# Performance work log

Hardware: AMD Instinct MI355X
Metric: run time of the kernel (lower is better)

Reference implementation:

```python
import jax, jax.numpy as jnp
import numpy as np

N_NODES = 100000
N_EDGES = 3200000
N_CLASSES = 16
P = 2  # p-norm order


def setup_inputs() -> dict:
    key = jax.random.key(0)
    k1, k2, k3 = jax.random.split(key, 3)
    edge_index = jax.random.randint(k1, (2, N_EDGES), 0, N_NODES, dtype=jnp.int64)
    edge_weights = jax.random.uniform(k2, (N_EDGES,), dtype=jnp.float32)
    y = jax.random.normal(k3, (N_NODES, N_CLASSES), dtype=jnp.float32)
    return {"edge_index": edge_index, "edge_weights": edge_weights, "y": y}


def reference(edge_index, edge_weights, y):
    row, col = edge_index[0], edge_index[1]
    n = y.shape[0]
    # sym normalization: degree = row-sum of weighted adjacency (O(E) segment sum,
    # replacing the original dense NxN materialization)
    degree = jax.ops.segment_sum(edge_weights, row, num_segments=n)
    d = jnp.sqrt(degree)
    d_r = d[row][:, None]  # (E,1)
    d_c = d[col][:, None]
    diff = y[row] / d_r - y[col] / d_c  # (E,C)
    pnorm = jnp.sum(jnp.abs(diff) ** P, axis=1) ** (1.0 / P)  # (E,)
    return jnp.mean(pnorm * edge_weights)
```

## Files before the change

### kernel.cpp

```cpp
#include <hip/hip_runtime.h>
#include <hip/hip_fp16.h>

#define N_NODES   100000
#define N_CLASSES 16
#define N_EDGES   3200000

#define R_DYN     3
#define NPR_DYN   33334
#define DYN_BYTES (NPR_DYN * 4)
#define S_DYN     85
#define EPS_DYN   37648

#define R_ST      8
#define NPR_ST    12500
#define S_ST      64
#define EPS_ST    50000

#define B_DEG     1024
#define KE        8

#define P_SHADOW  8
#define N_PAD     100416
#define KD        10


__device__ __forceinline__ unsigned f2fp8(float f) {
    unsigned u = __float_as_uint(f);
    unsigned s = (u >> 24) & 0x80u;
    float g = fabsf(f) * 0x1p-120f;
    unsigned gu = __float_as_uint(g);
    gu += 0x7FFFFu + ((gu >> 20) & 1u);
    unsigned mag = gu >> 20;
    if (mag > 0x7Eu) mag = 0x7Eu;
    return s | mag;
}

__device__ __forceinline__ float fp82f(unsigned b) {
    unsigned u = ((b & 0x80u) << 24) | ((b & 0x7Fu) << 20);
    return __uint_as_float(u) * 0x1p120f;
}

__device__ __forceinline__ float ssd4(unsigned a, unsigned b) {
    float s = 0.0f;
#pragma unroll
    for (int i = 0; i < 4; ++i) {
        float va = fp82f((a >> (8 * i)) & 0xFFu);
        float vb = fp82f((b >> (8 * i)) & 0xFFu);
        float d = va - vb;
        s += d * d;
    }
    return s;
}


__global__ __launch_bounds__(B_DEG) void lap_degree_dyn(
        const int* __restrict__ rows, const float* __restrict__ w,
        __half* __restrict__ shadows) {
    extern __shared__ float hist[];
    const int r   = blockIdx.x % R_DYN;
    const int s   = blockIdx.x / R_DYN;
    const int lo  = r * NPR_DYN;
    const int hi  = (lo + NPR_DYN < N_NODES) ? lo + NPR_DYN : N_NODES;
    const int cnt = hi - lo;

    for (int i = threadIdx.x; i < cnt; i += B_DEG) hist[i] = 0.0f;
    __syncthreads();

    const int base = s * EPS_DYN;
    for (int g = threadIdx.x; g < EPS_DYN / 4; g += B_DEG) {
        const int e = base + g * 4;
        if (e >= N_EDGES) continue;
        int4   r4 = *(const int4*)(rows + e);
        float4 w4 = *(const float4*)(w + e);
        int t;
        t = r4.x - lo; if ((unsigned)t < (unsigned)cnt) atomicAdd(&hist[t], w4.x);
        t = r4.y - lo; if ((unsigned)t < (unsigned)cnt) atomicAdd(&hist[t], w4.y);
        t = r4.z - lo; if ((unsigned)t < (unsigned)cnt) atomicAdd(&hist[t], w4.z);
        t = r4.w - lo; if ((unsigned)t < (unsigned)cnt) atomicAdd(&hist[t], w4.w);
    }
    __syncthreads();

    __half* dst = shadows + (size_t)s * N_NODES + lo;
    for (int i = threadIdx.x; i < cnt; i += B_DEG) dst[i] = __float2half(hist[i]);
}


__global__ __launch_bounds__(B_DEG) void lap_degree_static(
        const int* __restrict__ rows, const float* __restrict__ w,
        __half* __restrict__ shadows) {
    __shared__ float hist[NPR_ST];
    const int r  = blockIdx.x & (R_ST - 1);
    const int s  = blockIdx.x >> 3;
    const int lo = r * NPR_ST;

    for (int i = threadIdx.x; i < NPR_ST; i += B_DEG) hist[i] = 0.0f;
    __syncthreads();

    const int base = s * EPS_ST;
    for (int g = threadIdx.x; g < EPS_ST / 4; g += B_DEG) {
        const int e = base + g * 4;
        int4   r4 = *(const int4*)(rows + e);
        float4 w4 = *(const float4*)(w + e);
        int t;
        t = r4.x - lo; if ((unsigned)t < (unsigned)NPR_ST) atomicAdd(&hist[t], w4.x);
        t = r4.y - lo; if ((unsigned)t < (unsigned)NPR_ST) atomicAdd(&hist[t], w4.y);
        t = r4.z - lo; if ((unsigned)t < (unsigned)NPR_ST) atomicAdd(&hist[t], w4.z);
        t = r4.w - lo; if ((unsigned)t < (unsigned)NPR_ST) atomicAdd(&hist[t], w4.w);
    }
    __syncthreads();

    __half* dst = shadows + (size_t)s * N_NODES + lo;
    for (int i = threadIdx.x; i < NPR_ST; i += B_DEG) dst[i] = __float2half(hist[i]);
}


__global__ void lap_yhat_super(const __half* __restrict__ shadows,
                               const float* __restrict__ y,
                               unsigned char* __restrict__ yhat, int S) {
    const int n = blockIdx.x * blockDim.x + threadIdx.x;
    if (n >= N_NODES) return;
    float deg = 0.0f;
    for (int s = 0; s < S; ++s) deg += __half2float(shadows[(size_t)s * N_NODES + n]);
    const float inv = rsqrtf(deg);

    const float4* yr = (const float4*)(y + (size_t)n * N_CLASSES);
    uint4 o;
    unsigned* op = (unsigned*)&o;
#pragma unroll
    for (int j = 0; j < 4; ++j) {
        float4 v = yr[j];
        op[j] =  f2fp8(v.x * inv)
              | (f2fp8(v.y * inv) << 8)
              | (f2fp8(v.z * inv) << 16)
              | (f2fp8(v.w * inv) << 24);
    }
    *(uint4*)(yhat + (size_t)n * N_CLASSES) = o;
}


__global__ void lap_degree_p(const int* __restrict__ rows,
                             const float* __restrict__ w,
                             float* __restrict__ degp) {
    const int tid = blockIdx.x * blockDim.x + threadIdx.x;
    float* mydeg = degp + (size_t)(blockIdx.x & (P_SHADOW - 1)) * N_PAD;
    int   r[KD];
    float wv[KD];
#pragma unroll
    for (int k = 0; k < KD; ++k) {
        int e = tid + k * (N_EDGES / KD);
        r[k]  = rows[e];
        wv[k] = w[e];
    }
#pragma unroll
    for (int k = 0; k < KD; ++k) atomicAdd(&mydeg[r[k]], wv[k]);
}

__global__ void lap_yhat_mid(const float* __restrict__ degp,
                             const float* __restrict__ y,
                             unsigned char* __restrict__ yhat) {
    const int n = blockIdx.x * blockDim.x + threadIdx.x;
    if (n >= N_NODES) return;
    float deg = 0.0f;
#pragma unroll
    for (int p = 0; p < P_SHADOW; ++p) deg += degp[(size_t)p * N_PAD + n];
    const float inv = rsqrtf(deg);
    const float4* yr = (const float4*)(y + (size_t)n * N_CLASSES);
    uint4 o;
    unsigned* op = (unsigned*)&o;
#pragma unroll
    for (int j = 0; j < 4; ++j) {
        float4 v = yr[j];
        op[j] =  f2fp8(v.x * inv)
              | (f2fp8(v.y * inv) << 8)
              | (f2fp8(v.z * inv) << 16)
              | (f2fp8(v.w * inv) << 24);
    }
    *(uint4*)(yhat + (size_t)n * N_CLASSES) = o;
}


__global__ void lap_edge_fp8(const int* __restrict__ rows,
                             const int* __restrict__ cols,
                             const float* __restrict__ w,
                             const unsigned char* __restrict__ yhat,
                             float* __restrict__ out) {
    const int tid = blockIdx.x * blockDim.x + threadIdx.x;
    const long e0 = (long)tid * KE;
    float local = 0.0f;
    if (e0 < N_EDGES) {
        int4   ra = *(const int4*)(rows + e0);
        int4   rb = *(const int4*)(rows + e0 + 4);
        int4   ca = *(const int4*)(cols + e0);
        int4   cb = *(const int4*)(cols + e0 + 4);
        float4 wa = *(const float4*)(w + e0);
        float4 wb = *(const float4*)(w + e0 + 4);

        const int ri[KE] = {ra.x, ra.y, ra.z, ra.w, rb.x, rb.y, rb.z, rb.w};
        const int ci[KE] = {ca.x, ca.y, ca.z, ca.w, cb.x, cb.y, cb.z, cb.w};
        const float wv[KE] = {wa.x, wa.y, wa.z, wa.w, wb.x, wb.y, wb.z, wb.w};

        uint4 A[KE], B[KE];
#pragma unroll
        for (int k = 0; k < KE; ++k) {
            A[k] = *(const uint4*)(yhat + (size_t)ri[k] * N_CLASSES);
            B[k] = *(const uint4*)(yhat + (size_t)ci[k] * N_CLASSES);
        }
#pragma unroll
        for (int k = 0; k < KE; ++k) {
            float s = ssd4(A[k].x, B[k].x) + ssd4(A[k].y, B[k].y)
                    + ssd4(A[k].z, B[k].z) + ssd4(A[k].w, B[k].w);
            local += wv[k] * sqrtf(s);
        }
    }
#pragma unroll
    for (int off = 32; off > 0; off >>= 1) local += __shfl_down(local, off, 64);
    __shared__ float sm[4];
    const int lane = threadIdx.x & 63;
    const int wid  = threadIdx.x >> 6;
    if (lane == 0) sm[wid] = local;
    __syncthreads();
    if (threadIdx.x == 0)
        atomicAdd(out, (sm[0] + sm[1] + sm[2] + sm[3]) * (1.0f / (float)N_EDGES));
}


__global__ void lap_degree_kernel(const int* __restrict__ rows,
                                  const float* __restrict__ w,
                                  float* __restrict__ degree) {
    int i = blockIdx.x * blockDim.x + threadIdx.x;
    if (i < N_EDGES) atomicAdd(&degree[rows[i]], w[i]);
}

__global__ void lap_invd_kernel(const float* __restrict__ degree,
                                float* __restrict__ invd) {
    int i = blockIdx.x * blockDim.x + threadIdx.x;
    if (i < N_NODES) invd[i] = rsqrtf(degree[i]);
}

__global__ void lap_edge_kernel(const int* __restrict__ rows,
                                const int* __restrict__ cols,
                                const float* __restrict__ w,
                                const float* __restrict__ y,
                                const float* __restrict__ invd,
                                float* __restrict__ out) {
    int i = blockIdx.x * blockDim.x + threadIdx.x;
    float local = 0.0f;
    if (i < N_EDGES) {
        int r = rows[i], c = cols[i];
        float dr = invd[r], dc = invd[c];
        const float4* yr = (const float4*)(y + (size_t)r * N_CLASSES);
        const float4* yc = (const float4*)(y + (size_t)c * N_CLASSES);
        float s = 0.0f;
#pragma unroll
        for (int j = 0; j < N_CLASSES / 4; ++j) {
            float4 a = yr[j], b = yc[j];
            float d0 = a.x * dr - b.x * dc;
            float d1 = a.y * dr - b.y * dc;
            float d2 = a.z * dr - b.z * dc;
            float d3 = a.w * dr - b.w * dc;
            s += d0 * d0 + d1 * d1 + d2 * d2 + d3 * d3;
        }
        local = w[i] * sqrtf(s);
    }
#pragma unroll
    for (int off = 32; off > 0; off >>= 1) local += __shfl_down(local, off, 64);
    __shared__ float sm[4];
    int lane = threadIdx.x & 63, wid = threadIdx.x >> 6;
    if (lane == 0) sm[wid] = local;
    __syncthreads();
    if (threadIdx.x == 0)
        atomicAdd(out, (sm[0] + sm[1] + sm[2] + sm[3]) * (1.0f / (float)N_EDGES));
}


extern "C" void kernel_launch(void* const* d_in, const int* in_sizes, int n_in,
                              void* d_out, int out_size, void* d_ws, size_t ws_size,
                              hipStream_t stream) {
    const int*   edge_index = (const int*)d_in[0];
    const float* w          = (const float*)d_in[1];
    const float* y          = (const float*)d_in[2];
    float*       out        = (float*)d_out;

    const int* rows = edge_index;
    const int* cols = edge_index + N_EDGES;
    const int  B = 256;

    const size_t sh_bytes   = (size_t)S_DYN * N_NODES * sizeof(__half);
    const size_t need_super = sh_bytes + (size_t)N_NODES * N_CLASSES;

    const size_t yhat_mid_off = (size_t)P_SHADOW * N_PAD * sizeof(float);
    const size_t need_mid     = yhat_mid_off + (size_t)N_NODES * N_CLASSES;

    const int edge_blocks = (N_EDGES / KE + B - 1) / B;

    hipMemsetAsync(d_out, 0, sizeof(float), stream);

    if (ws_size >= need_super) {
        __half*        shadows = (__half*)d_ws;
        unsigned char* yhat    = (unsigned char*)d_ws + sh_bytes;

        hipError_t attr_ok = hipFuncSetAttribute(
            reinterpret_cast<const void*>(lap_degree_dyn),
            hipFuncAttributeMaxDynamicSharedMemorySize, DYN_BYTES);

        if (attr_ok == hipSuccess) {
            lap_degree_dyn<<<R_DYN * S_DYN, B_DEG, DYN_BYTES, stream>>>(rows, w, shadows);
            lap_yhat_super<<<(N_NODES + B - 1) / B, B, 0, stream>>>(shadows, y, yhat, S_DYN);
        } else {
            lap_degree_static<<<R_ST * S_ST, B_DEG, 0, stream>>>(rows, w, shadows);
            lap_yhat_super<<<(N_NODES + B - 1) / B, B, 0, stream>>>(shadows, y, yhat, S_ST);
        }
        lap_edge_fp8<<<edge_blocks, B, 0, stream>>>(rows, cols, w, yhat, out);
    } else if (ws_size >= need_mid) {
        float*         degp = (float*)d_ws;
        unsigned char* yhat = (unsigned char*)d_ws + yhat_mid_off;

        hipMemsetAsync(d_ws, 0, yhat_mid_off, stream);
        lap_degree_p<<<(N_EDGES / KD) / B, B, 0, stream>>>(rows, w, degp);
        lap_yhat_mid<<<(N_NODES + B - 1) / B, B, 0, stream>>>(degp, y, yhat);
        lap_edge_fp8<<<edge_blocks, B, 0, stream>>>(rows, cols, w, yhat, out);
    } else {
        float* degree = (float*)d_ws;
        float* invd   = degree + N_NODES;
        hipMemsetAsync(d_ws, 0, (size_t)N_NODES * sizeof(float), stream);
        lap_degree_kernel<<<(N_EDGES + B - 1) / B, B, 0, stream>>>(rows, w, degree);
        lap_invd_kernel<<<(N_NODES + B - 1) / B, B, 0, stream>>>(degree, invd);
        lap_edge_kernel<<<(N_EDGES + B - 1) / B, B, 0, stream>>>(rows, cols, w, y, invd, out);
    }
}
```

Baseline: 164.0 us.

## Fuse degree, normalization and edge stages into one cooperative kernel

Merges the degree histogram, the fp8 yhat construction and the edge reduction into a single cooperative kernel of 255 blocks of 1024 threads, using grid.sync between stages. The output memset is folded into the kernel. This is meant to remove the memset and the launch gaps between the three kernels. In exchange, the yhat stage runs with only about 392 active threads per block, and the edge stage becomes a grid-stride loop at limited occupancy with one large block per CU. It also depends on cooperative launch support, falling back to the static path if that fails, and the mid-size workspace path is removed.

New measurement: 213.8 us. 30.4% more time.

```diff
diff --git a/kernel.cpp b/kernel.cpp
--- a/kernel.cpp
+++ b/kernel.cpp
@@ -1,27 +1,27 @@
 #include <hip/hip_runtime.h>
 #include <hip/hip_fp16.h>
+#include <hip/hip_cooperative_groups.h>
+
+namespace cg = cooperative_groups;
 
 #define N_NODES   100000
 #define N_CLASSES 16
 #define N_EDGES   3200000
 
+#define GRID_F    255
+#define B_F       1024
 #define R_DYN     3
 #define NPR_DYN   33334
 #define DYN_BYTES (NPR_DYN * 4)
 #define S_DYN     85
 #define EPS_DYN   37648
+#define KE        8
 
 #define R_ST      8
 #define NPR_ST    12500
 #define S_ST      64
 #define EPS_ST    50000
-
 #define B_DEG     1024
-#define KE        8
-
-#define P_SHADOW  8
-#define N_PAD     100416
-#define KD        10
 
 
 __device__ __forceinline__ unsigned f2fp8(float f) {
@@ -53,35 +53,115 @@
 }
 
 
-__global__ __launch_bounds__(B_DEG) void lap_degree_dyn(
-        const int* __restrict__ rows, const float* __restrict__ w,
-        __half* __restrict__ shadows) {
+__global__ __launch_bounds__(B_F) void lap_fused(
+        const int* __restrict__ rows, const int* __restrict__ cols,
+        const float* __restrict__ w, const float* __restrict__ y,
+        __half* __restrict__ shadows, unsigned char* __restrict__ yhat,
+        float* __restrict__ out) {
     extern __shared__ float hist[];
-    const int r   = blockIdx.x % R_DYN;
-    const int s   = blockIdx.x / R_DYN;
-    const int lo  = r * NPR_DYN;
-    const int hi  = (lo + NPR_DYN < N_NODES) ? lo + NPR_DYN : N_NODES;
-    const int cnt = hi - lo;
-
-    for (int i = threadIdx.x; i < cnt; i += B_DEG) hist[i] = 0.0f;
-    __syncthreads();
-
-    const int base = s * EPS_DYN;
-    for (int g = threadIdx.x; g < EPS_DYN / 4; g += B_DEG) {
-        const int e = base + g * 4;
-        if (e >= N_EDGES) continue;
-        int4   r4 = *(const int4*)(rows + e);
-        float4 w4 = *(const float4*)(w + e);
-        int t;
-        t = r4.x - lo; if ((unsigned)t < (unsigned)cnt) atomicAdd(&hist[t], w4.x);
-        t = r4.y - lo; if ((unsigned)t < (unsigned)cnt) atomicAdd(&hist[t], w4.y);
-        t = r4.z - lo; if ((unsigned)t < (unsigned)cnt) atomicAdd(&hist[t], w4.z);
-        t = r4.w - lo; if ((unsigned)t < (unsigned)cnt) atomicAdd(&hist[t], w4.w);
-    }
-    __syncthreads();
-
-    __half* dst = shadows + (size_t)s * N_NODES + lo;
-    for (int i = threadIdx.x; i < cnt; i += B_DEG) dst[i] = __float2half(hist[i]);
+    cg::grid_group grid = cg::this_grid();
+
+    {
+        const int b   = blockIdx.x;
+        const int r   = b % R_DYN;
+        const int s   = b / R_DYN;
+        const int lo  = r * NPR_DYN;
+        const int hi  = (lo + NPR_DYN < N_NODES) ? lo + NPR_DYN : N_NODES;
+        const int cnt = hi - lo;
+
+        if (b == 0 && threadIdx.x == 0) out[0] = 0.0f;
+
+        for (int i = threadIdx.x; i < cnt; i += B_F) hist[i] = 0.0f;
+        __syncthreads();
+
+        const int base = s * EPS_DYN;
+        for (int g = threadIdx.x; g < EPS_DYN / 4; g += B_F) {
+            const int e = base + g * 4;
+            if (e >= N_EDGES) continue;
+            int4   r4 = *(const int4*)(rows + e);
+            float4 w4 = *(const float4*)(w + e);
+            int t;
+            t = r4.x - lo; if ((unsigned)t < (unsigned)cnt) atomicAdd(&hist[t], w4.x);
+            t = r4.y - lo; if ((unsigned)t < (unsigned)cnt) atomicAdd(&hist[t], w4.y);
+            t = r4.z - lo; if ((unsigned)t < (unsigned)cnt) atomicAdd(&hist[t], w4.z);
+            t = r4.w - lo; if ((unsigned)t < (unsigned)cnt) atomicAdd(&hist[t], w4.w);
+        }
+        __syncthreads();
+
+        __half* dst = shadows + (size_t)s * N_NODES + lo;
+        for (int i = threadIdx.x; i < cnt; i += B_F) dst[i] = __float2half(hist[i]);
+    }
+
+    grid.sync();
+
+    {
+        const int nb = (N_NODES + GRID_F - 1) / GRID_F;
+        const int n  = blockIdx.x * nb + threadIdx.x;
+        if (threadIdx.x < nb && n < N_NODES) {
+            float deg = 0.0f;
+            for (int s = 0; s < S_DYN; ++s)
+                deg += __half2float(shadows[(size_t)s * N_NODES + n]);
+            const float inv = rsqrtf(deg);
+            const float4* yr = (const float4*)(y + (size_t)n * N_CLASSES);
+            uint4 o;
+            unsigned* op = (unsigned*)&o;
+#pragma unroll
+            for (int j = 0; j < 4; ++j) {
+                float4 v = yr[j];
+                op[j] =  f2fp8(v.x * inv)
+                      | (f2fp8(v.y * inv) << 8)
+                      | (f2fp8(v.z * inv) << 16)
+                      | (f2fp8(v.w * inv) << 24);
+            }
+            *(uint4*)(yhat + (size_t)n * N_CLASSES) = o;
+        }
+    }
+
+    grid.sync();
+
+    {
+        const int  tid     = blockIdx.x * B_F + threadIdx.x;
+        const long stride  = (long)GRID_F * B_F * KE;
+        float local = 0.0f;
+        for (long e0 = (long)tid * KE; e0 < N_EDGES; e0 += stride) {
+            int4   ra = *(const int4*)(rows + e0);
+            int4   rb = *(const int4*)(rows + e0 + 4);
+            int4   ca = *(const int4*)(cols + e0);
+            int4   cb = *(const int4*)(cols + e0 + 4);
+            float4 wa = *(const float4*)(w + e0);
+            float4 wb = *(const float4*)(w + e0 + 4);
+
+            const int ri[KE] = {ra.x, ra.y, ra.z, ra.w, rb.x, rb.y, rb.z, rb.w};
+            const int ci[KE] = {ca.x, ca.y, ca.z, ca.w, cb.x, cb.y, cb.z, cb.w};
+            const float wv[KE] = {wa.x, wa.y, wa.z, wa.w, wb.x, wb.y, wb.z, wb.w};
+
+            uint4 A[KE], B[KE];
+#pragma unroll
+            for (int k = 0; k < KE; ++k) {
+                A[k] = *(const uint4*)(yhat + (size_t)ri[k] * N_CLASSES);
+                B[k] = *(const uint4*)(yhat + (size_t)ci[k] * N_CLASSES);
+            }
+#pragma unroll
+            for (int k = 0; k < KE; ++k) {
+                float s = ssd4(A[k].x, B[k].x) + ssd4(A[k].y, B[k].y)
+                        + ssd4(A[k].z, B[k].z) + ssd4(A[k].w, B[k].w);
+                local += wv[k] * sqrtf(s);
+            }
+        }
+#pragma unroll
+        for (int off = 32; off > 0; off >>= 1) local += __shfl_down(local, off, 64);
+        __syncthreads();
+        const int lane = threadIdx.x & 63;
+        const int wid  = threadIdx.x >> 6;
+        if (lane == 0) hist[wid] = local;
+        __syncthreads();
+        if (threadIdx.x == 0) {
+            float t = 0.0f;
+#pragma unroll
+            for (int i = 0; i < B_F / 64; ++i) t += hist[i];
+            atomicAdd(out, t * (1.0f / (float)N_EDGES));
+        }
+    }
 }
 
 
@@ -113,7 +193,6 @@
     for (int i = threadIdx.x; i < NPR_ST; i += B_DEG) dst[i] = __float2half(hist[i]);
 }
 
-
 __global__ void lap_yhat_super(const __half* __restrict__ shadows,
                                const float* __restrict__ y,
                                unsigned char* __restrict__ yhat, int S) {
@@ -122,7 +201,6 @@
     float deg = 0.0f;
     for (int s = 0; s < S; ++s) deg += __half2float(shadows[(size_t)s * N_NODES + n]);
     const float inv = rsqrtf(deg);
-
     const float4* yr = (const float4*)(y + (size_t)n * N_CLASSES);
     uint4 o;
     unsigned* op = (unsigned*)&o;
@@ -136,48 +214,6 @@
     }
     *(uint4*)(yhat + (size_t)n * N_CLASSES) = o;
 }
-
-
-__global__ void lap_degree_p(const int* __restrict__ rows,
-                             const float* __restrict__ w,
-                             float* __restrict__ degp) {
-    const int tid = blockIdx.x * blockDim.x + threadIdx.x;
-    float* mydeg = degp + (size_t)(blockIdx.x & (P_SHADOW - 1)) * N_PAD;
-    int   r[KD];
-    float wv[KD];
-#pragma unroll
-    for (int k = 0; k < KD; ++k) {
-        int e = tid + k * (N_EDGES / KD);
-        r[k]  = rows[e];
-        wv[k] = w[e];
-    }
-#pragma unroll
-    for (int k = 0; k < KD; ++k) atomicAdd(&mydeg[r[k]], wv[k]);
-}
-
-__global__ void lap_yhat_mid(const float* __restrict__ degp,
-                             const float* __restrict__ y,
-                             unsigned char* __restrict__ yhat) {
-    const int n = blockIdx.x * blockDim.x + threadIdx.x;
-    if (n >= N_NODES) return;
-    float deg = 0.0f;
-#pragma unroll
-    for (int p = 0; p < P_SHADOW; ++p) deg += degp[(size_t)p * N_PAD + n];
-    const float inv = rsqrtf(deg);
-    const float4* yr = (const float4*)(y + (size_t)n * N_CLASSES);
-    uint4 o;
-    unsigned* op = (unsigned*)&o;
-#pragma unroll
-    for (int j = 0; j < 4; ++j) {
-        float4 v = yr[j];
-        op[j] =  f2fp8(v.x * inv)
-              | (f2fp8(v.y * inv) << 8)
-              | (f2fp8(v.z * inv) << 16)
-              | (f2fp8(v.w * inv) << 24);
-    }
-    *(uint4*)(yhat + (size_t)n * N_CLASSES) = o;
-}
-
 
 __global__ void lap_edge_fp8(const int* __restrict__ rows,
                              const int* __restrict__ cols,
@@ -223,7 +259,6 @@
         atomicAdd(out, (sm[0] + sm[1] + sm[2] + sm[3]) * (1.0f / (float)N_EDGES));
 }
 
-
 __global__ void lap_degree_kernel(const int* __restrict__ rows,
                                   const float* __restrict__ w,
                                   float* __restrict__ degree) {
@@ -288,40 +323,31 @@
     const size_t sh_bytes   = (size_t)S_DYN * N_NODES * sizeof(__half);
     const size_t need_super = sh_bytes + (size_t)N_NODES * N_CLASSES;
 
-    const size_t yhat_mid_off = (size_t)P_SHADOW * N_PAD * sizeof(float);
-    const size_t need_mid     = yhat_mid_off + (size_t)N_NODES * N_CLASSES;
-
-    const int edge_blocks = (N_EDGES / KE + B - 1) / B;
-
-    hipMemsetAsync(d_out, 0, sizeof(float), stream);
-
     if (ws_size >= need_super) {
         __half*        shadows = (__half*)d_ws;
         unsigned char* yhat    = (unsigned char*)d_ws + sh_bytes;
 
-        hipError_t attr_ok = hipFuncSetAttribute(
-            reinterpret_cast<const void*>(lap_degree_dyn),
+        hipError_t ok = hipFuncSetAttribute(
+            reinterpret_cast<const void*>(lap_fused),
             hipFuncAttributeMaxDynamicSharedMemorySize, DYN_BYTES);
 
-        if (attr_ok == hipSuccess) {
-            lap_degree_dyn<<<R_DYN * S_DYN, B_DEG, DYN_BYTES, stream>>>(rows, w, shadows);
-            lap_yhat_super<<<(N_NODES + B - 1) / B, B, 0, stream>>>(shadows, y, yhat, S_DYN);
-        } else {
+        if (ok == hipSuccess) {
+            void* args[] = {(void*)&rows, (void*)&cols, (void*)&w, (void*)&y,
+                            (void*)&shadows, (void*)&yhat, (void*)&out};
+            ok = hipLaunchCooperativeKernel(
+                reinterpret_cast<const void*>(lap_fused),
+                dim3(GRID_F), dim3(B_F), args, DYN_BYTES, stream);
+        }
+        if (ok != hipSuccess) {
+            hipMemsetAsync(d_out, 0, sizeof(float), stream);
             lap_degree_static<<<R_ST * S_ST, B_DEG, 0, stream>>>(rows, w, shadows);
             lap_yhat_super<<<(N_NODES + B - 1) / B, B, 0, stream>>>(shadows, y, yhat, S_ST);
-        }
-        lap_edge_fp8<<<edge_blocks, B, 0, stream>>>(rows, cols, w, yhat, out);
-    } else if (ws_size >= need_mid) {
-        float*         degp = (float*)d_ws;
-        unsigned char* yhat = (unsigned char*)d_ws + yhat_mid_off;
-
-        hipMemsetAsync(d_ws, 0, yhat_mid_off, stream);
-        lap_degree_p<<<(N_EDGES / KD) / B, B, 0, stream>>>(rows, w, degp);
-        lap_yhat_mid<<<(N_NODES + B - 1) / B, B, 0, stream>>>(degp, y, yhat);
-        lap_edge_fp8<<<edge_blocks, B, 0, stream>>>(rows, cols, w, yhat, out);
+            lap_edge_fp8<<<(N_EDGES / KE + B - 1) / B, B, 0, stream>>>(rows, cols, w, yhat, out);
+        }
     } else {
         float* degree = (float*)d_ws;
         float* invd   = degree + N_NODES;
+        hipMemsetAsync(d_out, 0, sizeof(float), stream);
         hipMemsetAsync(d_ws, 0, (size_t)N_NODES * sizeof(float), stream);
         lap_degree_kernel<<<(N_EDGES + B - 1) / B, B, 0, stream>>>(rows, w, degree);
         lap_invd_kernel<<<(N_NODES + B - 1) / B, B, 0, stream>>>(degree, invd);
```
